# Optimization experiments

Hardware: AMD Instinct MI355X
Metric: run time of the kernel (lower is better)

The kernel has to match this reference:

```python
import jax, jax.numpy as jnp
import numpy as np

NUM_HEADS = 8
NUM_GROUPS = 8
NUM_ITERATIONS = 3
DT = 0.1
EPS = 1e-5


def group_norm(x, scale, bias):
    # x: [B, C, H, W], GroupNorm(8, C)
    B, C, H, W = x.shape
    xg = x.reshape(B, NUM_GROUPS, C // NUM_GROUPS, H, W)
    mean = xg.mean(axis=(2, 3, 4), keepdims=True)
    var = xg.var(axis=(2, 3, 4), keepdims=True)
    xg = (xg - mean) * jax.lax.rsqrt(var + EPS)
    x = xg.reshape(B, C, H, W)
    return x * scale[None, :, None, None] + bias[None, :, None, None]


def setup_inputs() -> dict:
    key = jax.random.key(0)
    ks = jax.random.split(key, 4)
    B, C, H, W = 8, 512, 32, 32
    x = jax.random.normal(ks[0], (B, C, H, W), dtype=jnp.float32)
    qkv_w = jax.random.normal(ks[1], (3 * C, C), dtype=jnp.float32) * (1.0 / np.sqrt(C))
    proj_w = jax.random.normal(ks[2], (C, C), dtype=jnp.float32) * (1.0 / np.sqrt(C))
    inl_w = jax.random.normal(ks[3], (C, C), dtype=jnp.float32) * (1.0 / np.sqrt(C))
    return {
        "x": x,
        "gn_scale": jnp.ones((C,), jnp.float32),
        "gn_bias": jnp.zeros((C,), jnp.float32),
        "qkv_w": qkv_w,
        "qkv_b": jnp.zeros((3 * C,), jnp.float32),
        "proj_w": proj_w,
        "proj_b": jnp.zeros((C,), jnp.float32),
        "inl_w": inl_w,
        "inl_b": jnp.zeros((C,), jnp.float32),
    }


def reference(x, gn_scale, gn_bias, qkv_w, qkv_b, proj_w, proj_b, inl_w, inl_b):
    B, C, H, W = x.shape
    nh = NUM_HEADS
    hd = C // nh
    S = H * W

    h = group_norm(x, gn_scale, gn_bias)

    # 1x1 conv == channel matmul
    qkv = jnp.einsum('oc,bchw->bohw', qkv_w, h) + qkv_b[None, :, None, None]
    q, k, v = jnp.split(qkv, 3, axis=1)  # each [B, C, H, W]

    def to_heads(t):  # [B, C, H, W] -> [B, nh, S, hd]
        return t.reshape(B, nh, hd, S).transpose(0, 1, 3, 2)

    q, k, v = to_heads(q), to_heads(k), to_heads(v)

    scale = hd ** (-0.5)
    attn = jax.nn.softmax(jnp.einsum('bnsd,bntd->bnst', q, k) * scale, axis=-1)
    h = jnp.einsum('bnst,bntd->bnsd', attn, v)  # [B, nh, S, hd]

    # back to [B, S, C] for INL refinement
    h_flat = h.transpose(0, 1, 3, 2).reshape(B, C, S).transpose(0, 2, 1)

    # SimpleINLDynamics: iterative Euler refinement x <- x + dt * tanh(W x + b)
    def step(hf, _):
        hf = hf + DT * jnp.tanh(jnp.einsum('bsc,oc->bso', hf, inl_w) + inl_b)
        return hf, None
    h_flat, _ = jax.lax.scan(step, h_flat, None, length=NUM_ITERATIONS)

    h = h_flat.transpose(0, 2, 1).reshape(B, C, H, W)
    h = jnp.einsum('oc,bchw->bohw', proj_w, h) + proj_b[None, :, None, None]
    return x + h
```

## Files before the change

### kernel.cpp

```cpp
#include <hip/hip_runtime.h>
#include <math.h>

#define B_ 8
#define C_ 512
#define S_ 1024
#define HD 64
#define NHEADS 8
#define NGROUPS 8
#define DT_STEP 0.1f
#define EPS_GN 1e-5f
#define LOG2E 1.4426950408889634f

typedef __attribute__((ext_vector_type(8))) short bf16x8;
typedef __attribute__((ext_vector_type(4))) float f32x4;
typedef __attribute__((ext_vector_type(8))) unsigned short ushort8;
typedef __attribute__((ext_vector_type(4))) unsigned short ushort4_t;

static __device__ __forceinline__ unsigned short f2bf(float f) {
  unsigned int u = __builtin_bit_cast(unsigned int, f);
  u += 0x7fff + ((u >> 16) & 1);
  return (unsigned short)(u >> 16);
}

static __device__ __forceinline__ unsigned short f2bf_fast(float f) {
  unsigned int u = __builtin_bit_cast(unsigned int, f);
  return (unsigned short)((u + 0x8000u) >> 16);
}

static __device__ __forceinline__ float bf2f(unsigned short u) {
  unsigned int t = ((unsigned int)u) << 16;
  return __builtin_bit_cast(float, t);
}

static __device__ __forceinline__ float exp2_raw(float x) {
  return __builtin_amdgcn_exp2f(x);
}

static __device__ __forceinline__ float fast_tanh(float x) {
  float xc = fminf(fmaxf(x, -15.f), 15.f);
  float e = exp2_raw(xc * (2.0f * LOG2E));
  return (e - 1.f) / (e + 1.f);
}

static __device__ __forceinline__ void gload_lds16(const unsigned short* g, unsigned short* l) {
  __builtin_amdgcn_global_load_lds(
      (const __attribute__((address_space(1))) unsigned int*)g,
      (__attribute__((address_space(3))) unsigned int*)l, 16, 0, 0);
}

__global__ __launch_bounds__(256) void prep_kernel(
    const float* __restrict__ a, const float* __restrict__ b, const float* __restrict__ c,
    unsigned short* __restrict__ A, unsigned short* __restrict__ B, unsigned short* __restrict__ C,
    const float* __restrict__ x, float* __restrict__ gpart) {
  int bid = blockIdx.x;
  int tid = threadIdx.x;
  if (bid < 384) {
    int off = bid * 2048;
    int i = off + tid * 8;
    f32x4 v0 = *(const f32x4*)(a + i);
    f32x4 v1 = *(const f32x4*)(a + i + 4);
    ushort8 o;
    o[0] = f2bf(v0[0]); o[1] = f2bf(v0[1]); o[2] = f2bf(v0[2]); o[3] = f2bf(v0[3]);
    o[4] = f2bf(v1[0]); o[5] = f2bf(v1[1]); o[6] = f2bf(v1[2]); o[7] = f2bf(v1[3]);
    *(ushort8*)(A + i) = o;
    return;
  }
  if (bid < 640) {
    const float* src; unsigned short* dst; int off;
    if (bid < 512) { src = b; dst = B; off = (bid - 384) * 2048; }
    else { src = c; dst = C; off = (bid - 512) * 2048; }
    int i = off + tid * 8;
    f32x4 v0 = *(const f32x4*)(src + i);
    f32x4 v1 = *(const f32x4*)(src + i + 4);
    ushort8 o;
    o[0] = f2bf(v0[0]); o[1] = f2bf(v0[1]); o[2] = f2bf(v0[2]); o[3] = f2bf(v0[3]);
    o[4] = f2bf(v1[0]); o[5] = f2bf(v1[1]); o[6] = f2bf(v1[2]); o[7] = f2bf(v1[3]);
    int orow = i >> 9, cbase = i & 511;
    int dsti = (cbase >> 5) * 16384 + orow * 32 + (cbase & 31);
    *(ushort8*)(dst + dsti) = o;
    return;
  }
  int sbid = bid - 640;
  int bg = sbid >> 3, chunk = sbid & 7;
  const float* xp = x + (size_t)bg * 65536 + (size_t)chunk * 8192;
  float sum = 0.f, sq = 0.f;
  #pragma unroll
  for (int i = 0; i < 8; ++i) {
    f32x4 v = *(const f32x4*)(xp + i * 1024 + tid * 4);
    sum += v[0] + v[1] + v[2] + v[3];
    sq += v[0]*v[0] + v[1]*v[1] + v[2]*v[2] + v[3]*v[3];
  }
  #pragma unroll
  for (int off = 32; off >= 1; off >>= 1) {
    sum += __shfl_xor(sum, off, 64);
    sq  += __shfl_xor(sq, off, 64);
  }
  __shared__ float s1[4], s2[4];
  int wave = tid >> 6, lane = tid & 63;
  if (lane == 0) { s1[wave] = sum; s2[wave] = sq; }
  __syncthreads();
  if (tid == 0) {
    float S = s1[0] + s1[1] + s1[2] + s1[3];
    float Q = s2[0] + s2[1] + s2[2] + s2[3];
    gpart[bg * 16 + chunk * 2] = S;
    gpart[bg * 16 + chunk * 2 + 1] = Q;
  }
}

__global__ __launch_bounds__(256) void gn_apply_t(
    const float* __restrict__ x, const float* __restrict__ gpart,
    const float* __restrict__ scale, const float* __restrict__ bias,
    unsigned short* __restrict__ h_t) {
  int bid = blockIdx.x;
  int bg = bid >> 4, st = bid & 15;
  int b = bg >> 3, g = bg & 7;
  float S = 0.f, Q = 0.f;
  #pragma unroll
  for (int i = 0; i < 8; ++i) {
    S += gpart[bg * 16 + i * 2];
    Q += gpart[bg * 16 + i * 2 + 1];
  }
  float mean = S / 65536.f;
  float var = Q / 65536.f - mean * mean;
  float inv = rsqrtf(var + EPS_GN);

  int tid = threadIdx.x;
  int sl = tid >> 2;
  int cq = (tid & 3) * 16;
  float sA[16], sB[16];
  #pragma unroll
  for (int u = 0; u < 16; ++u) {
    float scv = scale[g * 64 + cq + u];
    sA[u] = inv * scv;
    sB[u] = bias[g * 64 + cq + u] - mean * inv * scv;
  }

  const float* xp = x + ((size_t)b * C_ + (size_t)g * 64) * S_;
  __shared__ float tile[64][65];
  #pragma unroll
  for (int it = 0; it < 16; ++it) {
    int lin = it * 256 + tid;
    int c = lin >> 6, s = lin & 63;
    tile[c][s] = xp[(size_t)c * S_ + st * 64 + s];
  }
  __syncthreads();
  unsigned short vals[16];
  #pragma unroll
  for (int u = 0; u < 16; ++u)
    vals[u] = f2bf_fast(tile[cq + u][sl] * sA[u] + sB[u]);
  unsigned short* dst = h_t + ((size_t)b * S_ + st * 64 + sl) * C_ + g * 64 + cq;
  ushort8 lo, hi;
  #pragma unroll
  for (int u = 0; u < 8; ++u) { lo[u] = vals[u]; hi[u] = vals[u + 8]; }
  *(ushort8*)dst = lo;
  *(ushort8*)(dst + 8) = hi;
}

template<int MB, int NB, int WMG, int WNG>
__device__ __forceinline__ void gemm_nt_core(
    const unsigned short* __restrict__ Ab,
    const unsigned short* __restrict__ Bb,
    unsigned short* ldsA, unsigned short* ldsB,
    f32x4* acc) {
  constexpr int TI = (MB / WMG) / 16;
  constexpr int TJ = (NB / WNG) / 16;
  constexpr int NQA = MB * 4 / 256;
  constexpr int NQB = NB * 4 / 256;
  const int K = 512;
  const int tid = threadIdx.x;
  const int w = tid >> 6, lane = tid & 63, quad = lane >> 4, l15 = lane & 15;
  const int wm = (WNG == 1) ? w : ((WMG == 1) ? 0 : (w >> 1));
  const int wn = (WNG == 1) ? 0 : ((WMG == 1) ? w : (w & 1));

  ushort8 apf[NQA], bpf[NQB];
  #pragma unroll
  for (int q = 0; q < NQA; ++q) {
    int c = q * 256 + tid;
    apf[q] = *(const ushort8*)(Ab + (size_t)(c >> 2) * K + (c & 3) * 8);
  }
  #pragma unroll
  for (int q = 0; q < NQB; ++q) {
    int c = q * 256 + tid;
    bpf[q] = *(const ushort8*)(Bb + (size_t)(c >> 2) * K + (c & 3) * 8);
  }

  for (int k0 = 0; k0 < K; k0 += 32) {
    __syncthreads();
    #pragma unroll
    for (int q = 0; q < NQA; ++q) {
      int c = q * 256 + tid;
      *(ushort8*)(ldsA + c * 8) = apf[q];
    }
    #pragma unroll
    for (int q = 0; q < NQB; ++q) {
      int c = q * 256 + tid;
      *(ushort8*)(ldsB + c * 8) = bpf[q];
    }
    __syncthreads();
    if (k0 + 32 < K) {
      #pragma unroll
      for (int q = 0; q < NQA; ++q) {
        int c = q * 256 + tid;
        apf[q] = *(const ushort8*)(Ab + (size_t)(c >> 2) * K + k0 + 32 + (c & 3) * 8);
      }
      #pragma unroll
      for (int q = 0; q < NQB; ++q) {
        int c = q * 256 + tid;
        bpf[q] = *(const ushort8*)(Bb + (size_t)(c >> 2) * K + k0 + 32 + (c & 3) * 8);
      }
    }
    bf16x8 af[TI], bfr[TJ];
    #pragma unroll
    for (int i = 0; i < TI; ++i)
      af[i] = *(const bf16x8*)(ldsA + (wm * (MB / WMG) + i * 16 + l15) * 32 + quad * 8);
    #pragma unroll
    for (int j = 0; j < TJ; ++j)
      bfr[j] = *(const bf16x8*)(ldsB + (wn * (NB / WNG) + j * 16 + l15) * 32 + quad * 8);
    #pragma unroll
    for (int i = 0; i < TI; ++i)
      #pragma unroll
      for (int j = 0; j < TJ; ++j)
        acc[i * TJ + j] = __builtin_amdgcn_mfma_f32_16x16x32_bf16(af[i], bfr[j], acc[i * TJ + j], 0, 0, 0);
  }
}

__global__ __launch_bounds__(256) void gemm_qkv_mfma(
    const unsigned short* __restrict__ Wbf, const unsigned short* __restrict__ h_t,
    const float* __restrict__ bias,
    unsigned short* __restrict__ Qt, unsigned short* __restrict__ Kt,
    unsigned short* __restrict__ Vt) {
  __shared__ __align__(16) unsigned short ldsA[128 * 32];
  __shared__ __align__(16) unsigned short ldsB[128 * 32];
  int b = blockIdx.z;
  int bm = blockIdx.y * 128, bn = blockIdx.x * 128;
  f32x4 acc[16];
  #pragma unroll
  for (int t = 0; t < 16; ++t) acc[t] = (f32x4){0.f, 0.f, 0.f, 0.f};
  gemm_nt_core<128, 128, 2, 2>(Wbf + (size_t)bm * 512,
                               h_t + ((size_t)b * S_ + bn) * 512, ldsA, ldsB, acc);
  int tid = threadIdx.x, w = tid >> 6, lane = tid & 63, quad = lane >> 4, l15 = lane & 15;
  int wm = w >> 1, wn = w & 1;
  int tensor = bm >> 9;
  float qscale = (tensor == 0) ? 0.125f * LOG2E : 1.0f;
  #pragma unroll
  for (int i = 0; i < 4; ++i) {
    #pragma unroll
    for (int j = 0; j < 4; ++j) {
      int m0 = bm + wm * 64 + i * 16 + quad * 4;
      int ng = bn + wn * 64 + j * 16 + l15;
      f32x4 v = acc[i * 4 + j];
      if (tensor < 2) {
        int head = (m0 >> 6) & 7, d0 = m0 & 63;
        ushort4_t pk;
        #pragma unroll
        for (int r = 0; r < 4; ++r) pk[r] = f2bf((v[r] + bias[m0 + r]) * qscale);
        unsigned short* dst = (tensor ? Kt : Qt) +
            (((size_t)(b * 8 + head) * S_ + ng) * 64 + d0);
        *(ushort4_t*)dst = pk;
      } else {
        #pragma unroll
        for (int r = 0; r < 4; ++r)
          Vt[(size_t)b * (C_ * S_) + (size_t)(m0 - 1024 + r) * S_ + ng] = f2bf(v[r] + bias[m0 + r]);
      }
    }
  }
}

__global__ __launch_bounds__(256) void attn_mfma(
    const unsigned short* __restrict__ Qt,
    const unsigned short* __restrict__ Kt,
    const unsigned short* __restrict__ Vt,
    unsigned short* __restrict__ hflat_bf) {
  int tid = threadIdx.x, wave = tid >> 6, lane = tid & 63;
  int quad = lane >> 4, l15 = lane & 15;
  int bid = blockIdx.x;
  int bn = bid & 63, sblk = bid >> 6, b = bn >> 3, n = bn & 7;
  int s0w = sblk * 128 + wave * 32;

  __shared__ unsigned short k_lds[64][72];
  __shared__ unsigned short v_lds[64][72];
  __shared__ unsigned short p_lds[4][2][16][72];

  const unsigned short* Kb = Kt + ((size_t)(b * 8 + n)) * S_ * 64;
  const unsigned short* Vb = Vt + ((size_t)b * C_ + n * 64) * S_;

  bf16x8 qa[2][2];
  #pragma unroll
  for (int g = 0; g < 2; ++g) {
    const unsigned short* Qb = Qt + (((size_t)(b * 8 + n)) * S_ + s0w + g * 16 + l15) * 64;
    qa[g][0] = *(const bf16x8*)(Qb + quad * 8);
    qa[g][1] = *(const bf16x8*)(Qb + 32 + quad * 8);
  }

  bf16x8 ones;
  #pragma unroll
  for (int j = 0; j < 8; ++j) ones[j] = (short)0x3F80;

  f32x4 o_acc[2][4];
  f32x4 l_acc[2];
  #pragma unroll
  for (int g = 0; g < 2; ++g) {
    l_acc[g] = (f32x4){0.f, 0.f, 0.f, 0.f};
    #pragma unroll
    for (int dc = 0; dc < 4; ++dc) o_acc[g][dc] = (f32x4){0.f, 0.f, 0.f, 0.f};
  }

  int row0 = tid >> 3, c80 = (tid & 7) * 8;
  int row1 = (tid + 256) >> 3, c81 = c80;

  ushort8 kreg[2], vreg[2];
  kreg[0] = *(const ushort8*)(Kb + (size_t)row0 * 64 + c80);
  kreg[1] = *(const ushort8*)(Kb + (size_t)row1 * 64 + c81);
  vreg[0] = *(const ushort8*)(Vb + (size_t)row0 * S_ + c80);
  vreg[1] = *(const ushort8*)(Vb + (size_t)row1 * S_ + c81);

  for (int t0 = 0; t0 < S_; t0 += 64) {
    __syncthreads();
    *(ushort8*)&k_lds[row0][c80] = kreg[0];
    *(ushort8*)&k_lds[row1][c81] = kreg[1];
    *(ushort8*)&v_lds[row0][c80] = vreg[0];
    *(ushort8*)&v_lds[row1][c81] = vreg[1];
    __syncthreads();
    if (t0 + 64 < S_) {
      int t1 = t0 + 64;
      kreg[0] = *(const ushort8*)(Kb + (size_t)(t1 + row0) * 64 + c80);
      kreg[1] = *(const ushort8*)(Kb + (size_t)(t1 + row1) * 64 + c81);
      vreg[0] = *(const ushort8*)(Vb + (size_t)row0 * S_ + t1 + c80);
      vreg[1] = *(const ushort8*)(Vb + (size_t)row1 * S_ + t1 + c81);
    }

    f32x4 sc[2][4];
    #pragma unroll
    for (int tc = 0; tc < 4; ++tc) {
      bf16x8 kb0 = *(const bf16x8*)&k_lds[tc * 16 + l15][quad * 8];
      bf16x8 kb1 = *(const bf16x8*)&k_lds[tc * 16 + l15][32 + quad * 8];
      #pragma unroll
      for (int g = 0; g < 2; ++g) {
        f32x4 c = {0.f, 0.f, 0.f, 0.f};
        c = __builtin_amdgcn_mfma_f32_16x16x32_bf16(kb0, qa[g][0], c, 0, 0, 0);
        sc[g][tc] = __builtin_amdgcn_mfma_f32_16x16x32_bf16(kb1, qa[g][1], c, 0, 0, 0);
      }
    }

    #pragma unroll
    for (int g = 0; g < 2; ++g)
      #pragma unroll
      for (int tc = 0; tc < 4; ++tc) {
        ushort4_t p4;
        #pragma unroll
        for (int r = 0; r < 4; ++r) p4[r] = f2bf_fast(exp2_raw(sc[g][tc][r]));
        *(ushort4_t*)&p_lds[wave][g][l15][tc * 16 + quad * 4] = p4;
      }

    bf16x8 pa[2][2];
    #pragma unroll
    for (int g = 0; g < 2; ++g) {
      pa[g][0] = *(const bf16x8*)&p_lds[wave][g][l15][quad * 8];
      pa[g][1] = *(const bf16x8*)&p_lds[wave][g][l15][32 + quad * 8];
      l_acc[g] = __builtin_amdgcn_mfma_f32_16x16x32_bf16(pa[g][0], ones, l_acc[g], 0, 0, 0);
      l_acc[g] = __builtin_amdgcn_mfma_f32_16x16x32_bf16(pa[g][1], ones, l_acc[g], 0, 0, 0);
    }
    #pragma unroll
    for (int dc = 0; dc < 4; ++dc) {
      bf16x8 vb0 = *(const bf16x8*)&v_lds[dc * 16 + l15][quad * 8];
      bf16x8 vb1 = *(const bf16x8*)&v_lds[dc * 16 + l15][32 + quad * 8];
      #pragma unroll
      for (int g = 0; g < 2; ++g) {
        o_acc[g][dc] = __builtin_amdgcn_mfma_f32_16x16x32_bf16(pa[g][0], vb0, o_acc[g][dc], 0, 0, 0);
        o_acc[g][dc] = __builtin_amdgcn_mfma_f32_16x16x32_bf16(pa[g][1], vb1, o_acc[g][dc], 0, 0, 0);
      }
    }
  }

  #pragma unroll
  for (int g = 0; g < 2; ++g) {
    float inv_l[4];
    #pragma unroll
    for (int r = 0; r < 4; ++r) inv_l[r] = 1.f / l_acc[g][r];
    #pragma unroll
    for (int dc = 0; dc < 4; ++dc) {
      #pragma unroll
      for (int r = 0; r < 4; ++r) {
        int s = s0w + g * 16 + quad * 4 + r;
        size_t idx = ((size_t)b * S_ + s) * C_ + n * 64 + dc * 16 + l15;
        hflat_bf[idx] = f2bf_fast(o_acc[g][dc][r] * inv_l[r]);
      }
    }
  }
}

__global__ __launch_bounds__(1024, 4) void inl_proj_chain(
    const unsigned short* __restrict__ hbf,
    const unsigned short* __restrict__ Wi2,
    const unsigned short* __restrict__ Wp2,
    const float* __restrict__ ib, const float* __restrict__ pb,
    const float* __restrict__ x, float* __restrict__ Out) {
  __shared__ __align__(16) unsigned short h_lds[32][520];
  __shared__ __align__(16) unsigned short w_lds[2][16384];

  int tid = threadIdx.x;
  int wave = tid >> 6, lane = tid & 63, quad = lane >> 4, l15 = lane & 15;
  int wo = wave * 32;
  int bid = blockIdx.x;
  int b = bid >> 5, s0 = (bid & 31) * 32;

  const unsigned short* hsrc = hbf + (size_t)bid * 16384;
  ushort8 hv0 = *(const ushort8*)(hsrc + (size_t)tid * 8);
  ushort8 hv1 = *(const ushort8*)(hsrc + (size_t)(1024 + tid) * 8);

  float bi0 = ib[wo + l15], bi1 = ib[wo + 16 + l15];
  float bp0 = pb[wo + l15], bp1 = pb[wo + 16 + l15];

  *(ushort8*)&h_lds[tid >> 6][(tid & 63) * 8] = hv0;
  { int lin = 1024 + tid; *(ushort8*)&h_lds[lin >> 6][(lin & 63) * 8] = hv1; }

  f32x4 acc00 = {0.f,0.f,0.f,0.f}, acc01 = {0.f,0.f,0.f,0.f};
  f32x4 acc10 = {0.f,0.f,0.f,0.f}, acc11 = {0.f,0.f,0.f,0.f};

  const int o0 = wo + l15, o1 = wo + 16 + l15;
  const int wofs = wave * 1024;
  const int lofs = lane * 8;

  __syncthreads();

#define ISSUE_(g, buf) { \
    const unsigned short* ws_ = (((g) < 48) ? Wi2 : Wp2) + ((g) & 15) * 16384 + wofs; \
    gload_lds16(ws_ + lofs, &w_lds[buf][wofs]); \
    gload_lds16(ws_ + 512 + lofs, &w_lds[buf][wofs + 512]); }

  ISSUE_(0, 0);

  for (int g = 0; g < 64; ++g) {
    int cur = g & 1;
    asm volatile("s_waitcnt lgkmcnt(0)" ::: "memory");
    if (g + 1 < 64) {
      ISSUE_(g + 1, cur ^ 1);
      asm volatile("s_waitcnt vmcnt(2)" ::: "memory");
    } else {
      asm volatile("s_waitcnt vmcnt(0)" ::: "memory");
    }

    int kb = (g & 15) * 32 + quad * 8;
    bf16x8 a0 = *(const bf16x8*)&h_lds[l15][kb];
    bf16x8 a1 = *(const bf16x8*)&h_lds[16 + l15][kb];
    bf16x8 na = *(const bf16x8*)&w_lds[cur][o0 * 32 + quad * 8];
    bf16x8 nb = *(const bf16x8*)&w_lds[cur][o1 * 32 + quad * 8];
    acc00 = __builtin_amdgcn_mfma_f32_16x16x32_bf16(a0, na, acc00, 0, 0, 0);
    acc10 = __builtin_amdgcn_mfma_f32_16x16x32_bf16(a1, na, acc10, 0, 0, 0);
    acc01 = __builtin_amdgcn_mfma_f32_16x16x32_bf16(a0, nb, acc01, 0, 0, 0);
    acc11 = __builtin_amdgcn_mfma_f32_16x16x32_bf16(a1, nb, acc11, 0, 0, 0);

    if ((g & 15) == 15 && g < 63) {
      __syncthreads();
      #pragma unroll
      for (int r = 0; r < 4; ++r) {
        int sa = quad * 4 + r, sb = 16 + quad * 4 + r;
        h_lds[sa][o0] = f2bf_fast(bf2f(h_lds[sa][o0]) + DT_STEP * fast_tanh(acc00[r] + bi0));
        h_lds[sa][o1] = f2bf_fast(bf2f(h_lds[sa][o1]) + DT_STEP * fast_tanh(acc01[r] + bi1));
        h_lds[sb][o0] = f2bf_fast(bf2f(h_lds[sb][o0]) + DT_STEP * fast_tanh(acc10[r] + bi0));
        h_lds[sb][o1] = f2bf_fast(bf2f(h_lds[sb][o1]) + DT_STEP * fast_tanh(acc11[r] + bi1));
      }
      acc00 = (f32x4){0.f,0.f,0.f,0.f}; acc01 = (f32x4){0.f,0.f,0.f,0.f};
      acc10 = (f32x4){0.f,0.f,0.f,0.f}; acc11 = (f32x4){0.f,0.f,0.f,0.f};
      __syncthreads();
    }
  }

  {
    size_t base0 = (((size_t)b * 512 + o0) << 10) + (size_t)(s0 + quad * 4);
    size_t base1 = (((size_t)b * 512 + o1) << 10) + (size_t)(s0 + quad * 4);
    f32x4 xv, ov;
    xv = *(const f32x4*)(x + base0);
    #pragma unroll
    for (int r = 0; r < 4; ++r) ov[r] = xv[r] + bp0 + acc00[r];
    *(f32x4*)(Out + base0) = ov;
    xv = *(const f32x4*)(x + base0 + 16);
    #pragma unroll
    for (int r = 0; r < 4; ++r) ov[r] = xv[r] + bp0 + acc10[r];
    *(f32x4*)(Out + base0 + 16) = ov;
    xv = *(const f32x4*)(x + base1);
    #pragma unroll
    for (int r = 0; r < 4; ++r) ov[r] = xv[r] + bp1 + acc01[r];
    *(f32x4*)(Out + base1) = ov;
    xv = *(const f32x4*)(x + base1 + 16);
    #pragma unroll
    for (int r = 0; r < 4; ++r) ov[r] = xv[r] + bp1 + acc11[r];
    *(f32x4*)(Out + base1 + 16) = ov;
  }
#undef ISSUE_
}

extern "C" void kernel_launch(void* const* d_in, const int* in_sizes, int n_in,
                              void* d_out, int out_size, void* d_ws, size_t ws_size,
                              hipStream_t stream) {
  const float* x        = (const float*)d_in[0];
  const float* gn_scale = (const float*)d_in[1];
  const float* gn_bias  = (const float*)d_in[2];
  const float* qkv_w    = (const float*)d_in[3];
  const float* qkv_b    = (const float*)d_in[4];
  const float* proj_w   = (const float*)d_in[5];
  const float* proj_b   = (const float*)d_in[6];
  const float* inl_w    = (const float*)d_in[7];
  const float* inl_b    = (const float*)d_in[8];
  float* out = (float*)d_out;
  float* ws = (float*)d_ws;

  unsigned short* Qt  = (unsigned short*)(ws + 8388608);
  unsigned short* Kt  = (unsigned short*)(ws + 10485760);
  unsigned short* Vt  = (unsigned short*)(ws + 12582912);
  unsigned short* h_t = (unsigned short*)(ws + 14680064);
  unsigned short* Abf = (unsigned short*)(ws + 16777216);
  float* gpart = ws + 18874368;
  unsigned short* qkvw_bf  = (unsigned short*)(ws + 18878464);
  unsigned short* inlw_bf  = qkvw_bf + 786432;
  unsigned short* projw_bf = inlw_bf + 262144;

  prep_kernel<<<1152, 256, 0, stream>>>(qkv_w, inl_w, proj_w, qkvw_bf, inlw_bf, projw_bf, x, gpart);
  gn_apply_t<<<1024, 256, 0, stream>>>(x, gpart, gn_scale, gn_bias, h_t);
  gemm_qkv_mfma<<<dim3(8, 12, 8), 256, 0, stream>>>(qkvw_bf, h_t, qkv_b, Qt, Kt, Vt);
  attn_mfma<<<512, 256, 0, stream>>>(Qt, Kt, Vt, Abf);
  inl_proj_chain<<<256, 1024, 0, stream>>>(Abf, inlw_bf, projw_bf, inl_b, proj_b, x, out);
}
```

Baseline: 184.6 us.

## Halve waves per block in INL chain, widen per-wave tile, swizzle weight LDS

The fused INL+projection kernel now runs 8 waves per block instead of 16, each wave computing 64 output channels with eight accumulators, so every loaded h fragment feeds more MFMAs. The weight-prep kernel writes bf16 weight slabs with an XOR swizzle on 8-element chunks, and the kernel reads them with the matching swizzled column to cut LDS bank conflicts. The k-loop is fully unrolled over the four Euler/projection stages. In exchange there are fewer waves to hide load latency, more register pressure, and a longer unrolled body.

```diff
diff --git a/kernel.cpp b/kernel.cpp
--- a/kernel.cpp
+++ b/kernel.cpp
@@ -76,7 +76,8 @@
     o[0] = f2bf(v0[0]); o[1] = f2bf(v0[1]); o[2] = f2bf(v0[2]); o[3] = f2bf(v0[3]);
     o[4] = f2bf(v1[0]); o[5] = f2bf(v1[1]); o[6] = f2bf(v1[2]); o[7] = f2bf(v1[3]);
     int orow = i >> 9, cbase = i & 511;
-    int dsti = (cbase >> 5) * 16384 + orow * 32 + (cbase & 31);
+    int chunk = ((cbase & 31) >> 3) ^ ((orow >> 1) & 3);
+    int dsti = (cbase >> 5) * 16384 + orow * 32 + chunk * 8;
     *(ushort8*)(dst + dsti) = o;
     return;
   }
@@ -389,7 +390,7 @@
   }
 }
 
-__global__ __launch_bounds__(1024, 4) void inl_proj_chain(
+__global__ __launch_bounds__(512, 2) void inl_proj_chain(
     const unsigned short* __restrict__ hbf,
     const unsigned short* __restrict__ Wi2,
     const unsigned short* __restrict__ Wp2,
@@ -400,93 +401,119 @@
 
   int tid = threadIdx.x;
   int wave = tid >> 6, lane = tid & 63, quad = lane >> 4, l15 = lane & 15;
-  int wo = wave * 32;
+  int wo = wave * 64;
   int bid = blockIdx.x;
   int b = bid >> 5, s0 = (bid & 31) * 32;
 
   const unsigned short* hsrc = hbf + (size_t)bid * 16384;
   ushort8 hv0 = *(const ushort8*)(hsrc + (size_t)tid * 8);
-  ushort8 hv1 = *(const ushort8*)(hsrc + (size_t)(1024 + tid) * 8);
-
-  float bi0 = ib[wo + l15], bi1 = ib[wo + 16 + l15];
-  float bp0 = pb[wo + l15], bp1 = pb[wo + 16 + l15];
+  ushort8 hv1 = *(const ushort8*)(hsrc + (size_t)(512 + tid) * 8);
+  ushort8 hv2 = *(const ushort8*)(hsrc + (size_t)(1024 + tid) * 8);
+  ushort8 hv3 = *(const ushort8*)(hsrc + (size_t)(1536 + tid) * 8);
+
+  float bi0 = ib[wo + l15],      bi1 = ib[wo + 16 + l15];
+  float bi2 = ib[wo + 32 + l15], bi3 = ib[wo + 48 + l15];
+  float bp0 = pb[wo + l15],      bp1 = pb[wo + 16 + l15];
+  float bp2 = pb[wo + 32 + l15], bp3 = pb[wo + 48 + l15];
 
   *(ushort8*)&h_lds[tid >> 6][(tid & 63) * 8] = hv0;
-  { int lin = 1024 + tid; *(ushort8*)&h_lds[lin >> 6][(lin & 63) * 8] = hv1; }
+  { int lin = 512 + tid;  *(ushort8*)&h_lds[lin >> 6][(lin & 63) * 8] = hv1; }
+  { int lin = 1024 + tid; *(ushort8*)&h_lds[lin >> 6][(lin & 63) * 8] = hv2; }
+  { int lin = 1536 + tid; *(ushort8*)&h_lds[lin >> 6][(lin & 63) * 8] = hv3; }
 
   f32x4 acc00 = {0.f,0.f,0.f,0.f}, acc01 = {0.f,0.f,0.f,0.f};
+  f32x4 acc02 = {0.f,0.f,0.f,0.f}, acc03 = {0.f,0.f,0.f,0.f};
   f32x4 acc10 = {0.f,0.f,0.f,0.f}, acc11 = {0.f,0.f,0.f,0.f};
-
-  const int o0 = wo + l15, o1 = wo + 16 + l15;
-  const int wofs = wave * 1024;
+  f32x4 acc12 = {0.f,0.f,0.f,0.f}, acc13 = {0.f,0.f,0.f,0.f};
+
+  const int o0 = wo + l15,      o1 = wo + 16 + l15;
+  const int o2 = wo + 32 + l15, o3 = wo + 48 + l15;
+  const int wofs = wave * 2048;
   const int lofs = lane * 8;
+  const int wcol = (quad ^ ((l15 >> 1) & 3)) * 8;
 
   __syncthreads();
 
-#define ISSUE_(g, buf) { \
-    const unsigned short* ws_ = (((g) < 48) ? Wi2 : Wp2) + ((g) & 15) * 16384 + wofs; \
+#define ISSUE_(base, slab, buf) { \
+    const unsigned short* ws_ = (base) + (slab) * 16384 + wofs; \
     gload_lds16(ws_ + lofs, &w_lds[buf][wofs]); \
-    gload_lds16(ws_ + 512 + lofs, &w_lds[buf][wofs + 512]); }
-
-  ISSUE_(0, 0);
-
-  for (int g = 0; g < 64; ++g) {
-    int cur = g & 1;
-    asm volatile("s_waitcnt lgkmcnt(0)" ::: "memory");
-    if (g + 1 < 64) {
-      ISSUE_(g + 1, cur ^ 1);
-      asm volatile("s_waitcnt vmcnt(2)" ::: "memory");
-    } else {
-      asm volatile("s_waitcnt vmcnt(0)" ::: "memory");
-    }
-
-    int kb = (g & 15) * 32 + quad * 8;
-    bf16x8 a0 = *(const bf16x8*)&h_lds[l15][kb];
-    bf16x8 a1 = *(const bf16x8*)&h_lds[16 + l15][kb];
-    bf16x8 na = *(const bf16x8*)&w_lds[cur][o0 * 32 + quad * 8];
-    bf16x8 nb = *(const bf16x8*)&w_lds[cur][o1 * 32 + quad * 8];
-    acc00 = __builtin_amdgcn_mfma_f32_16x16x32_bf16(a0, na, acc00, 0, 0, 0);
-    acc10 = __builtin_amdgcn_mfma_f32_16x16x32_bf16(a1, na, acc10, 0, 0, 0);
-    acc01 = __builtin_amdgcn_mfma_f32_16x16x32_bf16(a0, nb, acc01, 0, 0, 0);
-    acc11 = __builtin_amdgcn_mfma_f32_16x16x32_bf16(a1, nb, acc11, 0, 0, 0);
-
-    if ((g & 15) == 15 && g < 63) {
+    gload_lds16(ws_ + 512 + lofs, &w_lds[buf][wofs + 512]); \
+    gload_lds16(ws_ + 1024 + lofs, &w_lds[buf][wofs + 1024]); \
+    gload_lds16(ws_ + 1536 + lofs, &w_lds[buf][wofs + 1536]); }
+
+  ISSUE_(Wi2, 0, 0);
+
+  #pragma unroll
+  for (int step = 0; step < 4; ++step) {
+    #pragma unroll
+    for (int s = 0; s < 16; ++s) {
+      const int g = step * 16 + s;
+      const int cur = g & 1;
+      asm volatile("s_waitcnt lgkmcnt(0)" ::: "memory");
+      if (g + 1 < 64) {
+        const unsigned short* nb_ = ((g + 1) < 48) ? Wi2 : Wp2;
+        ISSUE_(nb_, (g + 1) & 15, cur ^ 1);
+        asm volatile("s_waitcnt vmcnt(4)" ::: "memory");
+      } else {
+        asm volatile("s_waitcnt vmcnt(0)" ::: "memory");
+      }
+
+      const int kb = s * 32 + quad * 8;
+      bf16x8 a0 = *(const bf16x8*)&h_lds[l15][kb];
+      bf16x8 a1 = *(const bf16x8*)&h_lds[16 + l15][kb];
+      bf16x8 w0 = *(const bf16x8*)&w_lds[cur][o0 * 32 + wcol];
+      bf16x8 w1 = *(const bf16x8*)&w_lds[cur][o1 * 32 + wcol];
+      bf16x8 w2 = *(const bf16x8*)&w_lds[cur][o2 * 32 + wcol];
+      bf16x8 w3 = *(const bf16x8*)&w_lds[cur][o3 * 32 + wcol];
+      acc00 = __builtin_amdgcn_mfma_f32_16x16x32_bf16(a0, w0, acc00, 0, 0, 0);
+      acc10 = __builtin_amdgcn_mfma_f32_16x16x32_bf16(a1, w0, acc10, 0, 0, 0);
+      acc01 = __builtin_amdgcn_mfma_f32_16x16x32_bf16(a0, w1, acc01, 0, 0, 0);
+      acc11 = __builtin_amdgcn_mfma_f32_16x16x32_bf16(a1, w1, acc11, 0, 0, 0);
+      acc02 = __builtin_amdgcn_mfma_f32_16x16x32_bf16(a0, w2, acc02, 0, 0, 0);
+      acc12 = __builtin_amdgcn_mfma_f32_16x16x32_bf16(a1, w2, acc12, 0, 0, 0);
+      acc03 = __builtin_amdgcn_mfma_f32_16x16x32_bf16(a0, w3, acc03, 0, 0, 0);
+      acc13 = __builtin_amdgcn_mfma_f32_16x16x32_bf16(a1, w3, acc13, 0, 0, 0);
+    }
+
+    if (step < 3) {
       __syncthreads();
       #pragma unroll
       for (int r = 0; r < 4; ++r) {
         int sa = quad * 4 + r, sb = 16 + quad * 4 + r;
         h_lds[sa][o0] = f2bf_fast(bf2f(h_lds[sa][o0]) + DT_STEP * fast_tanh(acc00[r] + bi0));
         h_lds[sa][o1] = f2bf_fast(bf2f(h_lds[sa][o1]) + DT_STEP * fast_tanh(acc01[r] + bi1));
+        h_lds[sa][o2] = f2bf_fast(bf2f(h_lds[sa][o2]) + DT_STEP * fast_tanh(acc02[r] + bi2));
+        h_lds[sa][o3] = f2bf_fast(bf2f(h_lds[sa][o3]) + DT_STEP * fast_tanh(acc03[r] + bi3));
         h_lds[sb][o0] = f2bf_fast(bf2f(h_lds[sb][o0]) + DT_STEP * fast_tanh(acc10[r] + bi0));
         h_lds[sb][o1] = f2bf_fast(bf2f(h_lds[sb][o1]) + DT_STEP * fast_tanh(acc11[r] + bi1));
+        h_lds[sb][o2] = f2bf_fast(bf2f(h_lds[sb][o2]) + DT_STEP * fast_tanh(acc12[r] + bi2));
+        h_lds[sb][o3] = f2bf_fast(bf2f(h_lds[sb][o3]) + DT_STEP * fast_tanh(acc13[r] + bi3));
       }
       acc00 = (f32x4){0.f,0.f,0.f,0.f}; acc01 = (f32x4){0.f,0.f,0.f,0.f};
+      acc02 = (f32x4){0.f,0.f,0.f,0.f}; acc03 = (f32x4){0.f,0.f,0.f,0.f};
       acc10 = (f32x4){0.f,0.f,0.f,0.f}; acc11 = (f32x4){0.f,0.f,0.f,0.f};
+      acc12 = (f32x4){0.f,0.f,0.f,0.f}; acc13 = (f32x4){0.f,0.f,0.f,0.f};
       __syncthreads();
     }
   }
 
-  {
-    size_t base0 = (((size_t)b * 512 + o0) << 10) + (size_t)(s0 + quad * 4);
-    size_t base1 = (((size_t)b * 512 + o1) << 10) + (size_t)(s0 + quad * 4);
-    f32x4 xv, ov;
-    xv = *(const f32x4*)(x + base0);
-    #pragma unroll
-    for (int r = 0; r < 4; ++r) ov[r] = xv[r] + bp0 + acc00[r];
-    *(f32x4*)(Out + base0) = ov;
-    xv = *(const f32x4*)(x + base0 + 16);
-    #pragma unroll
-    for (int r = 0; r < 4; ++r) ov[r] = xv[r] + bp0 + acc10[r];
-    *(f32x4*)(Out + base0 + 16) = ov;
-    xv = *(const f32x4*)(x + base1);
-    #pragma unroll
-    for (int r = 0; r < 4; ++r) ov[r] = xv[r] + bp1 + acc01[r];
-    *(f32x4*)(Out + base1) = ov;
-    xv = *(const f32x4*)(x + base1 + 16);
-    #pragma unroll
-    for (int r = 0; r < 4; ++r) ov[r] = xv[r] + bp1 + acc11[r];
-    *(f32x4*)(Out + base1 + 16) = ov;
-  }
+#define EPI_(oj, bpj, aI0, aI1) { \
+    size_t base_ = (((size_t)b * 512 + (oj)) << 10) + (size_t)(s0 + quad * 4); \
+    f32x4 xv_, ov_; \
+    xv_ = *(const f32x4*)(x + base_); \
+    _Pragma("unroll") \
+    for (int r = 0; r < 4; ++r) ov_[r] = xv_[r] + (bpj) + aI0[r]; \
+    *(f32x4*)(Out + base_) = ov_; \
+    xv_ = *(const f32x4*)(x + base_ + 16); \
+    _Pragma("unroll") \
+    for (int r = 0; r < 4; ++r) ov_[r] = xv_[r] + (bpj) + aI1[r]; \
+    *(f32x4*)(Out + base_ + 16) = ov_; }
+
+  EPI_(o0, bp0, acc00, acc10);
+  EPI_(o1, bp1, acc01, acc11);
+  EPI_(o2, bp2, acc02, acc12);
+  EPI_(o3, bp3, acc03, acc13);
+#undef EPI_
 #undef ISSUE_
 }
 
@@ -519,5 +546,5 @@
   gn_apply_t<<<1024, 256, 0, stream>>>(x, gpart, gn_scale, gn_bias, h_t);
   gemm_qkv_mfma<<<dim3(8, 12, 8), 256, 0, stream>>>(qkvw_bf, h_t, qkv_b, Qt, Kt, Vt);
   attn_mfma<<<512, 256, 0, stream>>>(Qt, Kt, Vt, Abf);
-  inl_proj_chain<<<256, 1024, 0, stream>>>(Abf, inlw_bf, projw_bf, inl_b, proj_b, x, out);
-}
+  inl_proj_chain<<<256, 512, 0, stream>>>(Abf, inlw_bf, projw_bf, inl_b, proj_b, x, out);
+}
```

Result: no change. 183.4 us (median of 2 runs) (-0.6%).
